# Optimization experiments

Measured on AMD Instinct MI355X. Metric: run time of the kernel, lower is better.

## Reference

```python
import jax, jax.numpy as jnp
import numpy as np


def _quantize(x, weight):
    # x: (B, D, H, W); weight: (D, K)
    B, D, H, W = x.shape
    K = weight.shape[1]
    xf = x.reshape(B, D, H * W)  # (B, D, N)
    x2 = jnp.sum(xf * xf, axis=1)                      # (B, N)
    cross = jnp.einsum('bdn,dk->bnk', xf, weight)       # (B, N, K)
    e2 = jnp.sum(weight * weight, axis=0)               # (K,)
    d2 = x2[..., None] - 2.0 * cross + e2               # (B, N, K)
    argmin = jnp.argmin(d2, axis=-1)                    # (B, N)
    # gather codes: (B, N, D) -> (B, D, N) -> (B, D, H, W)
    quant = weight.T[argmin]                            # (B, N, D)
    result = jnp.transpose(quant, (0, 2, 1)).reshape(B, D, H, W)
    return result, argmin.reshape(B, H, W)


def setup_inputs() -> dict:
    key = jax.random.key(0)
    k1, k2 = jax.random.split(key)
    x = jax.random.normal(k1, (32, 256, 32, 32), dtype=jnp.float32)
    weight = jax.random.uniform(k2, (256, 512), dtype=jnp.float32)  # torch.rand init
    return {"x": x, "weight": weight}


def reference(x, weight):
    result, argmin = _quantize(x, weight)
    return result, argmin
```

## Files before the change

### kernel.cpp

```cpp
#include <hip/hip_runtime.h>

typedef __attribute__((ext_vector_type(8))) short bf16x8;
typedef __attribute__((ext_vector_type(16))) float f32x16;

__device__ __forceinline__ bool lex_lt(float av, int ai, float bv, int bi) {
  return av < bv || (av == bv && ai < bi);
}

__device__ __forceinline__ unsigned bf16_rne(float v) {
  unsigned u = __float_as_uint(v);
  return (u + 0x7fffu + ((u >> 16) & 1u)) >> 16;
}

__global__ __launch_bounds__(256) void vq_pre(
    const float* __restrict__ w, float* __restrict__ e2,
    short* __restrict__ wtil) {
  int blk = blockIdx.x;
  if (blk < 64) {
    int gid = blk * 256 + threadIdx.x;
    int n  = gid & 511;
    int kg = gid >> 9;
    bf16x8 hv, lv;
#pragma unroll
    for (int j = 0; j < 8; ++j) {
      float v = w[(kg * 8 + j) * 512 + n];
      unsigned h = bf16_rne(v);
      float hf = __uint_as_float(h << 16);
      unsigned l = bf16_rne(v - hf);
      hv[j] = (short)h;
      lv[j] = (short)l;
    }
    short* dst = wtil + (size_t)gid * 8;
    *(bf16x8*)dst = hv;
    *(bf16x8*)(dst + 131072) = lv;
  } else {
    int t = (blk - 64) * 256 + threadIdx.x;
    int k = t >> 2;
    int part = t & 3;
    double s = 0.0;
#pragma unroll 8
    for (int d = part * 64; d < part * 64 + 64; ++d) {
      double v = (double)w[d * 512 + k];
      s = fma(v, v, s);
    }
    s += __shfl_xor(s, 1);
    s += __shfl_xor(s, 2);
    if (part == 0) e2[k] = (float)s;
  }
}

__global__ __launch_bounds__(512, 4) void vq_main(
    const float* __restrict__ x, const float* __restrict__ w,
    const float* __restrict__ e2g, const short* __restrict__ wtil,
    float* __restrict__ out, float* __restrict__ arg_out) {
  __shared__ short xh[16384];
  __shared__ short xl[16384];
  __shared__ float e2s[512];
  __shared__ float tv1[512], tv2[512];
  __shared__ int   ti1[512], ti2[512];
  __shared__ int   pickS[64];

  const int tid = threadIdx.x;
  const int b  = blockIdx.x >> 4;
  const int n0 = (blockIdx.x & 15) << 6;
  const float* xbase = x + (size_t)b * 262144 + n0;

  {
    const int n4  = tid & 15;
    const int kg  = tid >> 4;
    float4 v[8];
#pragma unroll
    for (int j = 0; j < 8; ++j)
      v[j] = *(const float4*)(xbase + (size_t)(kg * 8 + j) * 1024 + (n4 << 2));
#pragma unroll
    for (int i = 0; i < 4; ++i) {
      int m = (n4 << 2) + i;
      bf16x8 hv, lv;
#pragma unroll
      for (int j = 0; j < 8; ++j) {
        float f = (i == 0) ? v[j].x : (i == 1) ? v[j].y : (i == 2) ? v[j].z : v[j].w;
        unsigned h = bf16_rne(f);
        unsigned l = bf16_rne(f - __uint_as_float(h << 16));
        hv[j] = (short)h;
        lv[j] = (short)l;
      }
      int off = (m << 8) + ((kg ^ (m & 7)) << 3);
      *(bf16x8*)&xh[off] = hv;
      *(bf16x8*)&xl[off] = lv;
    }
    if (tid < 512) e2s[tid] = e2g[tid];
  }
  __syncthreads();

  const int lane = tid & 63;
  const int wv   = tid >> 6;
  const int ln   = lane & 31;
  const int half = lane >> 5;
  const int wb   = wv << 6;

  f32x16 acc[2][2];
#pragma unroll
  for (int ct = 0; ct < 2; ++ct)
#pragma unroll
    for (int pt = 0; pt < 2; ++pt)
#pragma unroll
      for (int r = 0; r < 16; ++r) acc[ct][pt][r] = 0.f;

  const int m0 = ln, m1 = 32 + ln;
  const int a0base = m0 << 8, a1base = m1 << 8;
  const int a0sw = m0 & 7, a1sw = m1 & 7;

  size_t bofs[2];
#pragma unroll
  for (int ct = 0; ct < 2; ++ct) bofs[ct] = (size_t)((wb + (ct << 5) + ln) << 3);

  bf16x8 pch[2], pcl[2];
#pragma unroll
  for (int ct = 0; ct < 2; ++ct) {
    const short* p = wtil + ((size_t)half << 12) + bofs[ct];
    pch[ct] = *(const bf16x8*)p;
    pcl[ct] = *(const bf16x8*)(p + 131072);
  }

#pragma unroll
  for (int ch = 0; ch < 16; ++ch) {
    const int kg = (ch << 1) + half;
    bf16x8 xh0 = *(const bf16x8*)&xh[a0base + ((kg ^ a0sw) << 3)];
    bf16x8 xl0 = *(const bf16x8*)&xl[a0base + ((kg ^ a0sw) << 3)];
    bf16x8 xh1 = *(const bf16x8*)&xh[a1base + ((kg ^ a1sw) << 3)];
    bf16x8 xl1 = *(const bf16x8*)&xl[a1base + ((kg ^ a1sw) << 3)];
    bf16x8 cfh[2], cfl[2];
#pragma unroll
    for (int ct = 0; ct < 2; ++ct) { cfh[ct] = pch[ct]; cfl[ct] = pcl[ct]; }
    if (ch < 15) {
      const int kgn = ((ch + 1) << 1) + half;
#pragma unroll
      for (int ct = 0; ct < 2; ++ct) {
        const short* p = wtil + ((size_t)kgn << 12) + bofs[ct];
        pch[ct] = *(const bf16x8*)p;
        pcl[ct] = *(const bf16x8*)(p + 131072);
      }
    }
#pragma unroll
    for (int ct = 0; ct < 2; ++ct) {
      acc[ct][0] = __builtin_amdgcn_mfma_f32_32x32x16_bf16(cfh[ct], xh0, acc[ct][0], 0, 0, 0);
      acc[ct][0] = __builtin_amdgcn_mfma_f32_32x32x16_bf16(cfh[ct], xl0, acc[ct][0], 0, 0, 0);
      acc[ct][0] = __builtin_amdgcn_mfma_f32_32x32x16_bf16(cfl[ct], xh0, acc[ct][0], 0, 0, 0);
      acc[ct][1] = __builtin_amdgcn_mfma_f32_32x32x16_bf16(cfh[ct], xh1, acc[ct][1], 0, 0, 0);
      acc[ct][1] = __builtin_amdgcn_mfma_f32_32x32x16_bf16(cfh[ct], xl1, acc[ct][1], 0, 0, 0);
      acc[ct][1] = __builtin_amdgcn_mfma_f32_32x32x16_bf16(cfl[ct], xh1, acc[ct][1], 0, 0, 0);
    }
  }

  float e2r[2][16];
#pragma unroll
  for (int ct = 0; ct < 2; ++ct)
#pragma unroll
    for (int r = 0; r < 16; ++r)
      e2r[ct][r] = e2s[wb + (ct << 5) + (r & 3) + ((r >> 2) << 3) + (half << 2)];

#pragma unroll
  for (int pt = 0; pt < 2; ++pt) {
    float v1 = 3.4e38f, v2 = 3.4e38f;
    int i1 = 0x7fffffff, i2 = 0x7fffffff;
#pragma unroll
    for (int ct = 0; ct < 2; ++ct) {
#pragma unroll
      for (int r = 0; r < 16; ++r) {
        int k = wb + (ct << 5) + (r & 3) + ((r >> 2) << 3) + (half << 2);
        float s = fmaf(-2.f, acc[ct][pt][r], e2r[ct][r]);
        if (lex_lt(s, k, v1, i1)) { v2 = v1; i2 = i1; v1 = s; i1 = k; }
        else if (lex_lt(s, k, v2, i2)) { v2 = s; i2 = k; }
      }
    }
    {
      float ov1 = __shfl_xor(v1, 32);
      int   oi1 = __shfl_xor(i1, 32);
      float ov2 = __shfl_xor(v2, 32);
      int   oi2 = __shfl_xor(i2, 32);
      bool aFirst = lex_lt(v1, i1, ov1, oi1);
      float nv1 = aFirst ? v1 : ov1;  int ni1 = aFirst ? i1 : oi1;
      float cv  = aFirst ? ov1 : v1;  int ci  = aFirst ? oi1 : i1;
      float sv  = aFirst ? v2 : ov2;  int si  = aFirst ? i2 : oi2;
      bool cFirst = lex_lt(cv, ci, sv, si);
      v1 = nv1; i1 = ni1;
      v2 = cFirst ? cv : sv; i2 = cFirst ? ci : si;
    }
    if (half == 0) {
      int s = (wv << 6) + (pt << 5) + ln;
      tv1[s] = v1; ti1[s] = i1; tv2[s] = v2; ti2[s] = i2;
    }
  }
  __syncthreads();

  if (tid < 64) {
    int row = tid;
    float v1 = 3.4e38f, v2 = 3.4e38f;
    int i1 = 0x7fffffff, i2 = 0x7fffffff;
#pragma unroll
    for (int wvv = 0; wvv < 8; ++wvv) {
      int s = (wvv << 6) + row;
      float a1 = tv1[s]; int ai = ti1[s];
      float a2 = tv2[s]; int bi = ti2[s];
      if (lex_lt(a1, ai, v1, i1)) { v2 = v1; i2 = i1; v1 = a1; i1 = ai; }
      else if (lex_lt(a1, ai, v2, i2)) { v2 = a1; i2 = ai; }
      if (lex_lt(a2, bi, v1, i1)) { v2 = v1; i2 = i1; v1 = a2; i1 = bi; }
      else if (lex_lt(a2, bi, v2, i2)) { v2 = a2; i2 = bi; }
    }
    int pick = i1;
    if (v2 - v1 < 0.05f) {
      double s1 = 0.0, s2 = 0.0;
      const float* xp = x + (size_t)b * 262144 + n0 + row;
#pragma unroll 4
      for (int k = 0; k < 256; ++k) {
        double xv = (double)xp[(size_t)k * 1024];
        double w1 = (double)w[k * 512 + i1];
        double w2 = (double)w[k * 512 + i2];
        double t1 = xv - w1, t2 = xv - w2;
        s1 = fma(t1, t1, s1);
        s2 = fma(t2, t2, s2);
      }
      if (s2 < s1 || (s2 == s1 && i2 < i1)) pick = i2;
    }
    int p = b * 1024 + n0 + row;
    arg_out[p] = (float)pick;
    pickS[row] = pick;
  }
  __syncthreads();

  {
    const int nn0 = (tid & 15) << 2;
    const int d0g = tid >> 4;
    int pk0 = pickS[nn0], pk1 = pickS[nn0 + 1], pk2 = pickS[nn0 + 2], pk3 = pickS[nn0 + 3];
    float* obase = out + (size_t)b * 262144 + n0 + nn0;
#pragma unroll
    for (int dg = 0; dg < 8; ++dg) {
      int d = d0g + (dg << 5);
      const float* wr = w + d * 512;
      float4 o = make_float4(wr[pk0], wr[pk1], wr[pk2], wr[pk3]);
      *(float4*)(obase + (size_t)d * 1024) = o;
    }
  }
}

extern "C" void kernel_launch(void* const* d_in, const int* in_sizes, int n_in,
                              void* d_out, int out_size, void* d_ws, size_t ws_size,
                              hipStream_t stream) {
  const float* x = (const float*)d_in[0];
  const float* w = (const float*)d_in[1];
  float* out  = (float*)d_out;
  float* argf = out + 8388608;
  float* e2   = (float*)d_ws;
  short* wtil = (short*)(e2 + 512);

  vq_pre<<<72, 256, 0, stream>>>(w, e2, wtil);
  vq_main<<<512, 512, 0, stream>>>(x, w, e2, wtil, out, argf);
}
```

Before: 142.8 us.

## Gather codebook rows from transposed copy through shared memory for coalesced output

The pre-pass now also writes a transposed fp32 copy of the codebook into workspace when it is large enough. The main kernel gathers each picked code's contiguous row from that copy into padded shared memory, then writes the output with coalesced float4 stores. Before, each thread read scattered columns of the original weight. Shared memory becomes one reused arena so this staging needs no extra LDS. The fp64 refinement threshold for near ties is also tightened from 0.05 to 0.01, which cuts rescoring work but raises the risk of wrong argmin on close ties.

Result: faster. 137.1 us (-4.0%).

```diff
diff --git a/kernel.cpp b/kernel.cpp
--- a/kernel.cpp
+++ b/kernel.cpp
@@ -14,16 +14,18 @@
 
 __global__ __launch_bounds__(256) void vq_pre(
     const float* __restrict__ w, float* __restrict__ e2,
-    short* __restrict__ wtil) {
+    short* __restrict__ wtil, float* __restrict__ wT) {
   int blk = blockIdx.x;
   if (blk < 64) {
     int gid = blk * 256 + threadIdx.x;
     int n  = gid & 511;
     int kg = gid >> 9;
     bf16x8 hv, lv;
+    float vv[8];
 #pragma unroll
     for (int j = 0; j < 8; ++j) {
       float v = w[(kg * 8 + j) * 512 + n];
+      vv[j] = v;
       unsigned h = bf16_rne(v);
       float hf = __uint_as_float(h << 16);
       unsigned l = bf16_rne(v - hf);
@@ -33,6 +35,11 @@
     short* dst = wtil + (size_t)gid * 8;
     *(bf16x8*)dst = hv;
     *(bf16x8*)(dst + 131072) = lv;
+    if (wT) {
+      float* p = wT + (size_t)n * 256 + kg * 8;
+      *(float4*)p       = make_float4(vv[0], vv[1], vv[2], vv[3]);
+      *(float4*)(p + 4) = make_float4(vv[4], vv[5], vv[6], vv[7]);
+    }
   } else {
     int t = (blk - 64) * 256 + threadIdx.x;
     int k = t >> 2;
@@ -52,13 +59,17 @@
 __global__ __launch_bounds__(512, 4) void vq_main(
     const float* __restrict__ x, const float* __restrict__ w,
     const float* __restrict__ e2g, const short* __restrict__ wtil,
+    const float* __restrict__ wT,
     float* __restrict__ out, float* __restrict__ arg_out) {
-  __shared__ short xh[16384];
-  __shared__ short xl[16384];
-  __shared__ float e2s[512];
-  __shared__ float tv1[512], tv2[512];
-  __shared__ int   ti1[512], ti2[512];
-  __shared__ int   pickS[64];
+  __shared__ __align__(16) char arena[76032];
+  short* xh  = (short*)arena;
+  short* xl  = (short*)(arena + 32768);
+  float* e2s = (float*)(arena + 65536);
+  float* tv1 = (float*)(arena + 67584);
+  float* tv2 = (float*)(arena + 69632);
+  int*   ti1 = (int*)(arena + 71680);
+  int*   ti2 = (int*)(arena + 73728);
+  int*   pickS = (int*)(arena + 75776);
 
   const int tid = threadIdx.x;
   const int b  = blockIdx.x >> 4;
@@ -88,7 +99,7 @@
       *(bf16x8*)&xh[off] = hv;
       *(bf16x8*)&xl[off] = lv;
     }
-    if (tid < 512) e2s[tid] = e2g[tid];
+    e2s[tid & 511] = e2g[tid & 511];
   }
   __syncthreads();
 
@@ -208,7 +219,7 @@
       else if (lex_lt(a2, bi, v2, i2)) { v2 = a2; i2 = bi; }
     }
     int pick = i1;
-    if (v2 - v1 < 0.05f) {
+    if (v2 - v1 < 0.01f) {
       double s1 = 0.0, s2 = 0.0;
       const float* xp = x + (size_t)b * 262144 + n0 + row;
 #pragma unroll 4
@@ -228,7 +239,40 @@
   }
   __syncthreads();
 
-  {
+  if (wT) {
+    float* gbuf = (float*)arena;
+    {
+      const int pos  = tid >> 3;
+      const int dseg = tid & 7;
+      const float* wrow = wT + (size_t)pickS[pos] * 256;
+#pragma unroll
+      for (int j = 0; j < 8; ++j) {
+        float4 v = *(const float4*)(wrow + j * 32 + dseg * 4);
+        int base = pos * 265 + j * 33 + dseg * 4;
+        gbuf[base]     = v.x;
+        gbuf[base + 1] = v.y;
+        gbuf[base + 2] = v.z;
+        gbuf[base + 3] = v.w;
+      }
+    }
+    __syncthreads();
+    {
+      const int nn0 = (tid & 15) << 2;
+      const int d0g = tid >> 4;
+      float* obase = out + (size_t)b * 262144 + n0 + nn0;
+#pragma unroll
+      for (int dg = 0; dg < 8; ++dg) {
+        int d = d0g + (dg << 5);
+        int sa = (d >> 5) * 33 + (d & 31);
+        float4 o;
+        o.x = gbuf[(nn0 + 0) * 265 + sa];
+        o.y = gbuf[(nn0 + 1) * 265 + sa];
+        o.z = gbuf[(nn0 + 2) * 265 + sa];
+        o.w = gbuf[(nn0 + 3) * 265 + sa];
+        *(float4*)(obase + (size_t)d * 1024) = o;
+      }
+    }
+  } else {
     const int nn0 = (tid & 15) << 2;
     const int d0g = tid >> 4;
     int pk0 = pickS[nn0], pk1 = pickS[nn0 + 1], pk2 = pickS[nn0 + 2], pk3 = pickS[nn0 + 3];
@@ -251,8 +295,10 @@
   float* out  = (float*)d_out;
   float* argf = out + 8388608;
   float* e2   = (float*)d_ws;
-  short* wtil = (short*)(e2 + 512);
-
-  vq_pre<<<72, 256, 0, stream>>>(w, e2, wtil);
-  vq_main<<<512, 512, 0, stream>>>(x, w, e2, wtil, out, argf);
-}
+  short* wtil = (short*)((char*)d_ws + 2048);
+  size_t need = 2048 + 524288 + 524288;
+  float* wT   = (ws_size >= need) ? (float*)((char*)d_ws + 2048 + 524288) : nullptr;
+
+  vq_pre<<<72, 256, 0, stream>>>(w, e2, wtil, wT);
+  vq_main<<<512, 512, 0, stream>>>(x, w, e2, wtil, wT, out, argf);
+}
```
